# Performance work log

Measured on AMD Instinct MI355X. Metric: run time of the kernel, lower is better.

The kernel has to match this reference:

```python
import jax, jax.numpy as jnp
import numpy as np

B, S, D = 2, 2048, 1024
H = 16
HEAD_DIM = 64          # matches head_dim init arg; D // H == 64
HALF_WINDOW = 32       # local_window_size // 2
SCALE = HEAD_DIM ** -0.5


def setup_inputs() -> dict:
    key = jax.random.key(0)
    ks = jax.random.split(key, 6)
    std = 1.0 / np.sqrt(D)
    return {
        "x": jax.random.normal(ks[0], (B, S, D), dtype=jnp.float32),
        "Wq": jax.random.normal(ks[1], (D, D), dtype=jnp.float32) * std,
        "Wk": jax.random.normal(ks[2], (D, D), dtype=jnp.float32) * std,
        "Wv": jax.random.normal(ks[3], (D, D), dtype=jnp.float32) * std,
        "Wo": jax.random.normal(ks[4], (D, D), dtype=jnp.float32) * std,
        "bo": jnp.zeros((D,), dtype=jnp.float32),
    }


def reference(x, Wq, Wk, Wv, Wo, bo):
    b, s, d = x.shape
    h, hd = H, d // H

    def split_heads(y):  # [b, s, d] -> [b, h, s, hd]
        return y.reshape(b, s, h, hd).transpose(0, 2, 1, 3)

    q = split_heads(x @ Wq) * SCALE
    k = split_heads(x @ Wk)
    v = split_heads(x @ Wv)

    # dense scores [b, h, s, s] (module materializes full O(S^2) matrix)
    scores = jnp.einsum("bhqd,bhkd->bhqk", q, k)

    # local window |i-j| <= HALF_WINDOW combined with causal j <= i
    i = jnp.arange(s)
    local = jnp.abs(i[:, None] - i[None, :]) <= HALF_WINDOW
    causal = i[None, :] <= i[:, None]
    mask = local & causal  # [s, s]
    scores = jnp.where(mask[None, None, :, :], scores, -jnp.inf)

    attn = jax.nn.softmax(scores, axis=-1)  # diagonal always valid -> no NaN
    out = jnp.einsum("bhqk,bhkd->bhqd", attn, v)
    out = out.transpose(0, 2, 1, 3).reshape(b, s, d)  # merge heads
    return out @ Wo + bo
```

## Files before the change

### kernel.cpp

```cpp
#include <hip/hip_runtime.h>
#include <hip/hip_bf16.h>

typedef __bf16 bf16_t;
typedef __bf16 bf16x8 __attribute__((ext_vector_type(8)));
typedef __bf16 bf16x4 __attribute__((ext_vector_type(4)));
typedef float  f32x4  __attribute__((ext_vector_type(4)));

#define B_   2
#define S_   2048
#define D_   1024
#define H_   16
#define HD_  64
#define HW   32
#define SCALE_ 0.125f

__device__ __forceinline__ void gl_lds16(const bf16_t* g, bf16_t* l) {
  __builtin_amdgcn_global_load_lds(
      (const __attribute__((address_space(1))) void*)g,
      (__attribute__((address_space(3))) void*)l, 16, 0, 0);
}

__global__ __launch_bounds__(256) void k_conv(const float* __restrict__ X,
                                              const float* __restrict__ W0,
                                              const float* __restrict__ W1,
                                              const float* __restrict__ W2,
                                              const float* __restrict__ W3,
                                              bf16_t* __restrict__ Xb,
                                              bf16_t* __restrict__ Wt) {
  __shared__ bf16_t t[64][72];
  int bid = blockIdx.x;
  int tid = threadIdx.x;
  if (bid < 2048) {
    int i = bid * 256 + tid;
    const float4 a = ((const float4*)X)[i * 2];
    const float4 b = ((const float4*)X)[i * 2 + 1];
    bf16x8 r;
    r[0] = (bf16_t)a.x; r[1] = (bf16_t)a.y; r[2] = (bf16_t)a.z; r[3] = (bf16_t)a.w;
    r[4] = (bf16_t)b.x; r[5] = (bf16_t)b.y; r[6] = (bf16_t)b.z; r[7] = (bf16_t)b.w;
    ((bf16x8*)Xb)[i] = r;
    return;
  }
  int wb = bid - 2048;
  int wsel = wb >> 8;
  const float* W = (wsel == 0) ? W0 : (wsel == 1) ? W1 : (wsel == 2) ? W2 : W3;
  bf16_t* dst = Wt + (size_t)wsel * D_ * D_;
  int tile = wb & 255;
  int k0 = (tile >> 4) * 64, n0 = (tile & 15) * 64;
  int r = tid >> 4, c4 = (tid & 15) * 4;
#pragma unroll
  for (int i = 0; i < 4; ++i) {
    int row = i * 16 + r;
    float4 v = *(const float4*)(W + (size_t)(k0 + row) * D_ + n0 + c4);
    t[row][c4 + 0] = (bf16_t)v.x;
    t[row][c4 + 1] = (bf16_t)v.y;
    t[row][c4 + 2] = (bf16_t)v.z;
    t[row][c4 + 3] = (bf16_t)v.w;
  }
  __syncthreads();
#pragma unroll
  for (int i = 0; i < 4; ++i) {
    int row = i * 16 + r;
    bf16x4 o;
    o[0] = t[c4 + 0][row];
    o[1] = t[c4 + 1][row];
    o[2] = t[c4 + 2][row];
    o[3] = t[c4 + 3][row];
    *(bf16x4*)(dst + (size_t)(n0 + row) * D_ + k0 + c4) = o;
  }
}

__global__ __launch_bounds__(256) void k_gemm_qkv(const bf16_t* __restrict__ X,
                                                  const bf16_t* __restrict__ Wt,
                                                  bf16_t* __restrict__ Q,
                                                  bf16_t* __restrict__ K,
                                                  bf16_t* __restrict__ V) {
  __shared__ bf16_t sA[128 * 32];
  __shared__ bf16_t sB[128 * 32];
  int bid = blockIdx.x;
  int mt = bid & 31, nt = bid >> 5;
  int wsel = nt >> 3;
  int n0 = (nt & 7) * 128, m0 = mt * 128;
  const bf16_t* Wp = Wt + (size_t)wsel * D_ * D_;
  int tid = threadIdx.x, lane = tid & 63, wave = tid >> 6;
  int wr = (wave >> 1) * 64, wc = (wave & 1) * 64;
  int r0 = wave * 32 + (lane >> 2);
  int ce = (lane & 3) * 8;
  const bf16_t* gA0 = X + (size_t)(m0 + r0) * D_ + ce;
  const bf16_t* gB0 = Wp + (size_t)(n0 + r0) * D_ + ce;
  bf16_t* lA0 = sA + wave * 1024;
  bf16_t* lB0 = sB + wave * 1024;
  f32x4 acc[4][4] = {};
  int kq = (lane >> 4) * 8, rl = lane & 15;
  for (int kt = 0; kt < D_; kt += 32) {
    __syncthreads();
    gl_lds16(gA0 + kt, lA0);
    gl_lds16(gA0 + kt + (size_t)16 * D_, lA0 + 512);
    gl_lds16(gB0 + kt, lB0);
    gl_lds16(gB0 + kt + (size_t)16 * D_, lB0 + 512);
    __syncthreads();
    bf16x8 af[4], bfr[4];
#pragma unroll
    for (int m = 0; m < 4; ++m)
      af[m] = *(const bf16x8*)&sA[(wr + m * 16 + rl) * 32 + kq];
#pragma unroll
    for (int n = 0; n < 4; ++n)
      bfr[n] = *(const bf16x8*)&sB[(wc + n * 16 + rl) * 32 + kq];
#pragma unroll
    for (int m = 0; m < 4; ++m)
#pragma unroll
      for (int n = 0; n < 4; ++n)
        acc[m][n] = __builtin_amdgcn_mfma_f32_16x16x32_bf16(af[m], bfr[n], acc[m][n], 0, 0, 0);
  }
  float qscale = (wsel == 0) ? SCALE_ : 1.0f;
#pragma unroll
  for (int m = 0; m < 4; ++m) {
#pragma unroll
    for (int n = 0; n < 4; ++n) {
#pragma unroll
      for (int r = 0; r < 4; ++r) {
        int gm = m0 + wr + m * 16 + (lane >> 4) * 4 + r;
        int gn = n0 + wc + n * 16 + rl;
        int b = gm >> 11, s = gm & 2047;
        int h = gn >> 6, hd = gn & 63;
        bf16_t val = (bf16_t)(acc[m][n][r] * qscale);
        if (wsel == 0)
          Q[(((size_t)(b * H_ + h)) * S_ + s) * HD_ + hd] = val;
        else if (wsel == 1)
          K[(((size_t)(b * H_ + h)) * S_ + s) * HD_ + hd] = val;
        else
          V[(((size_t)(b * H_ + h)) * HD_ + hd) * S_ + s] = val;
      }
    }
  }
}

__global__ __launch_bounds__(256) void k_gemm_out(const bf16_t* __restrict__ A,
                                                  const bf16_t* __restrict__ Wp,
                                                  const float* __restrict__ bo,
                                                  float* __restrict__ out) {
  __shared__ bf16_t sA[64 * 32];
  __shared__ bf16_t sB[128 * 32];
  int bid = blockIdx.x;
  int mt = bid & 63, nt = bid >> 6;
  int n0 = nt * 128, m0 = mt * 64;
  int tid = threadIdx.x, lane = tid & 63, wave = tid >> 6;
  int wc = wave * 32;
  int crow = lane >> 2, ccol = (lane & 3) * 8;
  const bf16_t* gsrc0; bf16_t* ldst0;
  const bf16_t* gsrc1; bf16_t* ldst1;
  const bf16_t* gsrc2; bf16_t* ldst2;
#pragma unroll
  for (int j = 0; j < 3; ++j) {
    int c = wave * 3 + j;
    const bf16_t* g; bf16_t* l;
    if (c < 4) {
      g = A + (size_t)(m0 + c * 16 + crow) * D_ + ccol;
      l = sA + c * 512;
    } else {
      g = Wp + (size_t)(n0 + (c - 4) * 16 + crow) * D_ + ccol;
      l = sB + (c - 4) * 512;
    }
    if (j == 0) { gsrc0 = g; ldst0 = l; }
    else if (j == 1) { gsrc1 = g; ldst1 = l; }
    else { gsrc2 = g; ldst2 = l; }
  }
  f32x4 acc[4][2] = {};
  int kq = (lane >> 4) * 8, rl = lane & 15, hi = lane >> 4;
  for (int kt = 0; kt < D_; kt += 32) {
    __syncthreads();
    gl_lds16(gsrc0 + kt, ldst0);
    gl_lds16(gsrc1 + kt, ldst1);
    gl_lds16(gsrc2 + kt, ldst2);
    __syncthreads();
    bf16x8 af[4], bfr[2];
#pragma unroll
    for (int m = 0; m < 4; ++m)
      af[m] = *(const bf16x8*)&sA[(m * 16 + rl) * 32 + kq];
#pragma unroll
    for (int n = 0; n < 2; ++n)
      bfr[n] = *(const bf16x8*)&sB[(wc + n * 16 + rl) * 32 + kq];
#pragma unroll
    for (int m = 0; m < 4; ++m)
#pragma unroll
      for (int n = 0; n < 2; ++n)
        acc[m][n] = __builtin_amdgcn_mfma_f32_16x16x32_bf16(af[m], bfr[n], acc[m][n], 0, 0, 0);
  }
#pragma unroll
  for (int m = 0; m < 4; ++m) {
#pragma unroll
    for (int n = 0; n < 2; ++n) {
#pragma unroll
      for (int r = 0; r < 4; ++r) {
        int gm = m0 + m * 16 + hi * 4 + r;
        int gn = n0 + wc + n * 16 + rl;
        out[(size_t)gm * D_ + gn] = acc[m][n][r] + bo[gn];
      }
    }
  }
}

#define QB 64
#define KW 112
#define KLP 68
#define VTP 116

__global__ __launch_bounds__(256) void k_attn(const bf16_t* __restrict__ Q,
                                              const bf16_t* __restrict__ K,
                                              const bf16_t* __restrict__ Vt,
                                              bf16_t* __restrict__ O) {
  __shared__ bf16_t sK[KW][KLP];
  __shared__ bf16_t sV[HD_][VTP];
  __shared__ bf16_t sP[4][16][KLP];
  int bid = blockIdx.x;
  int qb = bid & 31, bh = bid >> 5;
  int q0 = qb * QB;
  const bf16_t* Kp = K + (size_t)bh * S_ * HD_;
  const bf16_t* Vp = Vt + (size_t)bh * HD_ * S_;
  const bf16_t* Qp = Q + (size_t)bh * S_ * HD_;
  int tid = threadIdx.x;
  int lane = tid & 63, wave = tid >> 6;
  int rl = lane & 15, hi = lane >> 4;
  int wk0b = q0 - HW;
  bf16x8 qf0 = *(const bf16x8*)(Qp + (size_t)(q0 + wave * 16 + rl) * HD_ + hi * 8);
  bf16x8 qf1 = *(const bf16x8*)(Qp + (size_t)(q0 + wave * 16 + rl) * HD_ + 32 + hi * 8);
  for (int idx = tid; idx < KW * 8; idx += 256) {
    int row = idx >> 3, c8 = (idx & 7) * 8;
    int kg = wk0b + row;
    kg = kg < 0 ? 0 : (kg > S_ - 1 ? S_ - 1 : kg);
    *(bf16x8*)&sK[row][c8] = *(const bf16x8*)(Kp + (size_t)kg * HD_ + c8);
  }
  for (int idx = tid; idx < HD_ * 14; idx += 256) {
    int row = idx / 14, c8 = (idx % 14) * 8;
    int ks = wk0b + c8;
    ks = ks < 0 ? 0 : (ks > S_ - 8 ? S_ - 8 : ks);
    *(bf16x8*)&sV[row][c8] = *(const bf16x8*)(Vp + (size_t)row * S_ + ks);
  }
  __syncthreads();
  int wko = wave * 16;
  f32x4 accs[4] = {};
#pragma unroll
  for (int kb = 0; kb < 4; ++kb) {
    bf16x8 kf = *(const bf16x8*)&sK[wko + kb * 16 + rl][hi * 8];
    accs[kb] = __builtin_amdgcn_mfma_f32_16x16x32_bf16(kf, qf0, accs[kb], 0, 0, 0);
  }
#pragma unroll
  for (int kb = 0; kb < 4; ++kb) {
    bf16x8 kf = *(const bf16x8*)&sK[wko + kb * 16 + rl][32 + hi * 8];
    accs[kb] = __builtin_amdgcn_mfma_f32_16x16x32_bf16(kf, qf1, accs[kb], 0, 0, 0);
  }
  float p[4][4];
  float mx = -1e30f;
#pragma unroll
  for (int kb = 0; kb < 4; ++kb) {
#pragma unroll
    for (int r = 0; r < 4; ++r) {
      int kl = kb * 16 + hi * 4 + r;
      bool valid = (kl >= rl) && (kl <= rl + HW) && (wk0b + wko + kl >= 0);
      float s = valid ? accs[kb][r] : -1e30f;
      p[kb][r] = s;
      mx = fmaxf(mx, s);
    }
  }
  mx = fmaxf(mx, __shfl_xor(mx, 16));
  mx = fmaxf(mx, __shfl_xor(mx, 32));
  float sum = 0.f;
#pragma unroll
  for (int kb = 0; kb < 4; ++kb)
#pragma unroll
    for (int r = 0; r < 4; ++r) {
      p[kb][r] = __expf(p[kb][r] - mx);
      sum += p[kb][r];
    }
  sum += __shfl_xor(sum, 16);
  sum += __shfl_xor(sum, 32);
  float inv = 1.f / sum;
#pragma unroll
  for (int kb = 0; kb < 4; ++kb) {
    bf16x4 pv;
#pragma unroll
    for (int r = 0; r < 4; ++r) pv[r] = (bf16_t)(p[kb][r] * inv);
    *(bf16x4*)&sP[wave][rl][kb * 16 + hi * 4] = pv;
  }
  f32x4 acco[4] = {};
#pragma unroll
  for (int ks = 0; ks < 2; ++ks) {
    bf16x8 aP = *(const bf16x8*)&sP[wave][rl][ks * 32 + hi * 8];
#pragma unroll
    for (int n = 0; n < 4; ++n) {
      bf16x8 bV = *(const bf16x8*)&sV[n * 16 + rl][wko + ks * 32 + hi * 8];
      acco[n] = __builtin_amdgcn_mfma_f32_16x16x32_bf16(aP, bV, acco[n], 0, 0, 0);
    }
  }
  int b = bh >> 4, h = bh & 15;
#pragma unroll
  for (int n = 0; n < 4; ++n) {
#pragma unroll
    for (int r = 0; r < 4; ++r) {
      int qgl = q0 + wave * 16 + hi * 4 + r;
      int d = n * 16 + rl;
      O[((size_t)(b * S_ + qgl)) * D_ + h * HD_ + d] = (bf16_t)acco[n][r];
    }
  }
}

extern "C" void kernel_launch(void* const* d_in, const int* in_sizes, int n_in,
                              void* d_out, int out_size, void* d_ws, size_t ws_size,
                              hipStream_t stream) {
  const float* x  = (const float*)d_in[0];
  const float* Wq = (const float*)d_in[1];
  const float* Wk = (const float*)d_in[2];
  const float* Wv = (const float*)d_in[3];
  const float* Wo = (const float*)d_in[4];
  const float* bo = (const float*)d_in[5];
  float* out = (float*)d_out;
  char* ws = (char*)d_ws;
  bf16_t* xb = (bf16_t*)(ws);
  bf16_t* wt = (bf16_t*)(ws + (size_t)(8 << 20));
  bf16_t* qb = (bf16_t*)(ws + (size_t)(16 << 20));
  bf16_t* kb = (bf16_t*)(ws + (size_t)(24 << 20));
  bf16_t* vb = (bf16_t*)(ws + (size_t)(32 << 20));
  bf16_t* ob = (bf16_t*)(ws + (size_t)(40 << 20));

  hipLaunchKernelGGL(k_conv, dim3(3072), dim3(256), 0, stream,
                     x, Wq, Wk, Wv, Wo, xb, wt);
  hipLaunchKernelGGL(k_gemm_qkv, dim3(768), dim3(256), 0, stream, xb, wt, qb, kb, vb);
  hipLaunchKernelGGL(k_attn, dim3(1024), dim3(256), 0, stream, qb, kb, vb, ob);
  hipLaunchKernelGGL(k_gemm_out, dim3(512), dim3(256), 0, stream,
                     ob, wt + (size_t)3 * D_ * D_, bo, out);
}
```

Measured before the change: 81.50 us.

## Rewrite QKV GEMM with triple-buffered async LDS pipeline and swizzled layout

The QKV projection GEMM moves to 512-thread blocks with 128x192 tiles spanning the fused Q/K/V weight, a K-step of 64, and a three-stage global-to-LDS async pipeline synchronised through explicit vmcnt waits and barriers. LDS rows are XOR-swizzled to avoid bank conflicts, and MFMA issue runs at raised wave priority. This targets exposed load latency and the two barriers per 32-wide K step of the old loop. In exchange it uses much more LDS (about 120KB), which limits blocks per CU, and the hand-coded waitcnt counts are fragile.

```diff
diff --git a/kernel.cpp b/kernel.cpp
--- a/kernel.cpp
+++ b/kernel.cpp
@@ -69,64 +69,107 @@
   }
 }
 
-__global__ __launch_bounds__(256) void k_gemm_qkv(const bf16_t* __restrict__ X,
+__global__ __launch_bounds__(512) void k_gemm_qkv(const bf16_t* __restrict__ X,
                                                   const bf16_t* __restrict__ Wt,
                                                   bf16_t* __restrict__ Q,
-                                                  bf16_t* __restrict__ K,
+                                                  bf16_t* __restrict__ Kb,
                                                   bf16_t* __restrict__ V) {
-  __shared__ bf16_t sA[128 * 32];
-  __shared__ bf16_t sB[128 * 32];
+  __shared__ bf16_t sA[3 * 128 * 64];
+  __shared__ bf16_t sB[3 * 192 * 64];
   int bid = blockIdx.x;
   int mt = bid & 31, nt = bid >> 5;
-  int wsel = nt >> 3;
-  int n0 = (nt & 7) * 128, m0 = mt * 128;
-  const bf16_t* Wp = Wt + (size_t)wsel * D_ * D_;
+  int m0 = mt * 128, n0g = nt * 192;
   int tid = threadIdx.x, lane = tid & 63, wave = tid >> 6;
-  int wr = (wave >> 1) * 64, wc = (wave & 1) * 64;
-  int r0 = wave * 32 + (lane >> 2);
-  int ce = (lane & 3) * 8;
-  const bf16_t* gA0 = X + (size_t)(m0 + r0) * D_ + ce;
-  const bf16_t* gB0 = Wp + (size_t)(n0 + r0) * D_ + ce;
-  bf16_t* lA0 = sA + wave * 1024;
-  bf16_t* lB0 = sB + wave * 1024;
-  f32x4 acc[4][4] = {};
-  int kq = (lane >> 4) * 8, rl = lane & 15;
-  for (int kt = 0; kt < D_; kt += 32) {
-    __syncthreads();
-    gl_lds16(gA0 + kt, lA0);
-    gl_lds16(gA0 + kt + (size_t)16 * D_, lA0 + 512);
-    gl_lds16(gB0 + kt, lB0);
-    gl_lds16(gB0 + kt + (size_t)16 * D_, lB0 + 512);
-    __syncthreads();
-    bf16x8 af[4], bfr[4];
-#pragma unroll
-    for (int m = 0; m < 4; ++m)
-      af[m] = *(const bf16x8*)&sA[(wr + m * 16 + rl) * 32 + kq];
-#pragma unroll
-    for (int n = 0; n < 4; ++n)
-      bfr[n] = *(const bf16x8*)&sB[(wc + n * 16 + rl) * 32 + kq];
-#pragma unroll
-    for (int m = 0; m < 4; ++m)
-#pragma unroll
-      for (int n = 0; n < 4; ++n)
-        acc[m][n] = __builtin_amdgcn_mfma_f32_16x16x32_bf16(af[m], bfr[n], acc[m][n], 0, 0, 0);
-  }
-  float qscale = (wsel == 0) ? SCALE_ : 1.0f;
+  int wm = wave >> 2, wn = wave & 3;
+  int srow8 = lane >> 3, sc16 = (lane & 7) ^ srow8;
+  int rl = lane & 15, hi = lane >> 4, r7 = rl & 7;
+  const bf16_t* gst0; const bf16_t* gst1; const bf16_t* gst2;
+  const bf16_t* gst3; const bf16_t* gst4;
+  int lst0, lst1, lst2, lst3, lst4;
+  {
+    int c0 = wave,     c1 = 8 + wave;
+    gst0 = X + (size_t)(m0 + c0 * 8 + srow8) * D_ + sc16 * 8;  lst0 = c0 * 512;
+    gst1 = X + (size_t)(m0 + c1 * 8 + srow8) * D_ + sc16 * 8;  lst1 = c1 * 512;
+    int b0 = wave, b1 = 8 + wave, b2 = 16 + wave;
+    gst2 = Wt + (size_t)(n0g + b0 * 8 + srow8) * D_ + sc16 * 8; lst2 = b0 * 512;
+    gst3 = Wt + (size_t)(n0g + b1 * 8 + srow8) * D_ + sc16 * 8; lst3 = b1 * 512;
+    gst4 = Wt + (size_t)(n0g + b2 * 8 + srow8) * D_ + sc16 * 8; lst4 = b2 * 512;
+  }
+#define STAGE_(bi, kt) do { \
+    gl_lds16(gst0 + (kt), sA + (bi) * 8192 + lst0);  \
+    gl_lds16(gst1 + (kt), sA + (bi) * 8192 + lst1);  \
+    gl_lds16(gst2 + (kt), sB + (bi) * 12288 + lst2); \
+    gl_lds16(gst3 + (kt), sB + (bi) * 12288 + lst3); \
+    gl_lds16(gst4 + (kt), sB + (bi) * 12288 + lst4); \
+  } while (0)
+  f32x4 acc[4][3] = {};
+  STAGE_(0, 0);
+  STAGE_(1, 64);
+  asm volatile("s_waitcnt vmcnt(5)" ::: "memory");
+  __builtin_amdgcn_sched_barrier(0);
+  __builtin_amdgcn_s_barrier();
+  asm volatile("" ::: "memory");
+  int cur = 0;
+  for (int t = 0; t < 16; ++t) {
+    const bf16_t* pA = sA + cur * 8192;
+    const bf16_t* pB = sB + cur * 12288;
+    bf16x8 af[4][2], bfr[3][2];
+#pragma unroll
+    for (int m = 0; m < 4; ++m) {
+      int rr = (wm * 64 + m * 16 + rl) * 64;
+#pragma unroll
+      for (int kk = 0; kk < 2; ++kk)
+        af[m][kk] = *(const bf16x8*)&pA[rr + ((kk * 4 + hi) ^ r7) * 8];
+    }
+#pragma unroll
+    for (int n = 0; n < 3; ++n) {
+      int rr = (wn * 48 + n * 16 + rl) * 64;
+#pragma unroll
+      for (int kk = 0; kk < 2; ++kk)
+        bfr[n][kk] = *(const bf16x8*)&pB[rr + ((kk * 4 + hi) ^ r7) * 8];
+    }
+    int sb = cur + 2; if (sb >= 3) sb -= 3;
+    if (t + 2 < 16) STAGE_(sb, (t + 2) * 64);
+    __builtin_amdgcn_s_setprio(1);
+#pragma unroll
+    for (int kk = 0; kk < 2; ++kk)
+#pragma unroll
+      for (int m = 0; m < 4; ++m)
+#pragma unroll
+        for (int n = 0; n < 3; ++n)
+          acc[m][n] = __builtin_amdgcn_mfma_f32_16x16x32_bf16(af[m][kk], bfr[n][kk], acc[m][n], 0, 0, 0);
+    __builtin_amdgcn_s_setprio(0);
+    if (t < 14) {
+      asm volatile("s_waitcnt vmcnt(5)" ::: "memory");
+    } else if (t == 14) {
+      asm volatile("s_waitcnt vmcnt(0)" ::: "memory");
+    }
+    if (t < 15) {
+      __builtin_amdgcn_sched_barrier(0);
+      __builtin_amdgcn_s_barrier();
+      asm volatile("" ::: "memory");
+    }
+    if (++cur == 3) cur = 0;
+  }
+#undef STAGE_
 #pragma unroll
   for (int m = 0; m < 4; ++m) {
-#pragma unroll
-    for (int n = 0; n < 4; ++n) {
+    int gm = m0 + wm * 64 + m * 16 + hi * 4;
+#pragma unroll
+    for (int n = 0; n < 3; ++n) {
+      int gn = n0g + wn * 48 + n * 16 + rl;
+      int wsel = gn >> 10, col = gn & 1023;
+      int h = col >> 6, hd = col & 63;
+      float qs = (wsel == 0) ? SCALE_ : 1.0f;
 #pragma unroll
       for (int r = 0; r < 4; ++r) {
-        int gm = m0 + wr + m * 16 + (lane >> 4) * 4 + r;
-        int gn = n0 + wc + n * 16 + rl;
-        int b = gm >> 11, s = gm & 2047;
-        int h = gn >> 6, hd = gn & 63;
-        bf16_t val = (bf16_t)(acc[m][n][r] * qscale);
+        int gmr = gm + r;
+        int b = gmr >> 11, s = gmr & 2047;
+        bf16_t val = (bf16_t)(acc[m][n][r] * qs);
         if (wsel == 0)
           Q[(((size_t)(b * H_ + h)) * S_ + s) * HD_ + hd] = val;
         else if (wsel == 1)
-          K[(((size_t)(b * H_ + h)) * S_ + s) * HD_ + hd] = val;
+          Kb[(((size_t)(b * H_ + h)) * S_ + s) * HD_ + hd] = val;
         else
           V[(((size_t)(b * H_ + h)) * HD_ + hd) * S_ + s] = val;
       }
@@ -323,7 +366,7 @@
 
   hipLaunchKernelGGL(k_conv, dim3(3072), dim3(256), 0, stream,
                      x, Wq, Wk, Wv, Wo, xb, wt);
-  hipLaunchKernelGGL(k_gemm_qkv, dim3(768), dim3(256), 0, stream, xb, wt, qb, kb, vb);
+  hipLaunchKernelGGL(k_gemm_qkv, dim3(512), dim3(512), 0, stream, xb, wt, qb, kb, vb);
   hipLaunchKernelGGL(k_attn, dim3(1024), dim3(256), 0, stream, qb, kb, vb, ob);
   hipLaunchKernelGGL(k_gemm_out, dim3(512), dim3(256), 0, stream,
                      ob, wt + (size_t)3 * D_ * D_, bo, out);
```

Result: slower. 83.56 us (+2.5%).

## Triple-buffer QKV GEMM LDS loads with async prefetch and one barrier per step

Applied to the files above, without the earlier changes.

The QKV projection GEMM now keeps three LDS stages and issues direct global-to-LDS loads two k-steps ahead. Per iteration it waits on vmcnt and uses a single barrier instead of two full syncthreads. MFMA issue is raised in priority with s_setprio. This aims to hide global-load latency behind MFMA work, at the cost of triple the LDS footprint (48KB per block), which may lower occupancy.

```diff
diff --git a/kernel.cpp b/kernel.cpp
--- a/kernel.cpp
+++ b/kernel.cpp
@@ -72,10 +72,10 @@
 __global__ __launch_bounds__(256) void k_gemm_qkv(const bf16_t* __restrict__ X,
                                                   const bf16_t* __restrict__ Wt,
                                                   bf16_t* __restrict__ Q,
-                                                  bf16_t* __restrict__ K,
+                                                  bf16_t* __restrict__ Kb,
                                                   bf16_t* __restrict__ V) {
-  __shared__ bf16_t sA[128 * 32];
-  __shared__ bf16_t sB[128 * 32];
+  __shared__ bf16_t sA[3 * 128 * 32];
+  __shared__ bf16_t sB[3 * 128 * 32];
   int bid = blockIdx.x;
   int mt = bid & 31, nt = bid >> 5;
   int wsel = nt >> 3;
@@ -87,30 +87,54 @@
   int ce = (lane & 3) * 8;
   const bf16_t* gA0 = X + (size_t)(m0 + r0) * D_ + ce;
   const bf16_t* gB0 = Wp + (size_t)(n0 + r0) * D_ + ce;
-  bf16_t* lA0 = sA + wave * 1024;
-  bf16_t* lB0 = sB + wave * 1024;
+  int lofs = wave * 1024;
+#define QSTAGE_(bi, kt) do { \
+    gl_lds16(gA0 + (kt), sA + (bi) * 4096 + lofs);        \
+    gl_lds16(gA0 + (kt) + (size_t)16 * D_, sA + (bi) * 4096 + lofs + 512); \
+    gl_lds16(gB0 + (kt), sB + (bi) * 4096 + lofs);        \
+    gl_lds16(gB0 + (kt) + (size_t)16 * D_, sB + (bi) * 4096 + lofs + 512); \
+  } while (0)
   f32x4 acc[4][4] = {};
   int kq = (lane >> 4) * 8, rl = lane & 15;
-  for (int kt = 0; kt < D_; kt += 32) {
-    __syncthreads();
-    gl_lds16(gA0 + kt, lA0);
-    gl_lds16(gA0 + kt + (size_t)16 * D_, lA0 + 512);
-    gl_lds16(gB0 + kt, lB0);
-    gl_lds16(gB0 + kt + (size_t)16 * D_, lB0 + 512);
-    __syncthreads();
+  QSTAGE_(0, 0);
+  QSTAGE_(1, 32);
+  asm volatile("s_waitcnt vmcnt(4)" ::: "memory");
+  __builtin_amdgcn_sched_barrier(0);
+  __builtin_amdgcn_s_barrier();
+  asm volatile("" ::: "memory");
+  int cur = 0;
+  for (int t = 0; t < 32; ++t) {
+    const bf16_t* pA = sA + cur * 4096;
+    const bf16_t* pB = sB + cur * 4096;
     bf16x8 af[4], bfr[4];
 #pragma unroll
     for (int m = 0; m < 4; ++m)
-      af[m] = *(const bf16x8*)&sA[(wr + m * 16 + rl) * 32 + kq];
+      af[m] = *(const bf16x8*)&pA[(wr + m * 16 + rl) * 32 + kq];
 #pragma unroll
     for (int n = 0; n < 4; ++n)
-      bfr[n] = *(const bf16x8*)&sB[(wc + n * 16 + rl) * 32 + kq];
+      bfr[n] = *(const bf16x8*)&pB[(wc + n * 16 + rl) * 32 + kq];
+    int sb = cur + 2; if (sb >= 3) sb -= 3;
+    if (t + 2 < 32) QSTAGE_(sb, (t + 2) * 32);
+    __builtin_amdgcn_s_setprio(1);
 #pragma unroll
     for (int m = 0; m < 4; ++m)
 #pragma unroll
       for (int n = 0; n < 4; ++n)
         acc[m][n] = __builtin_amdgcn_mfma_f32_16x16x32_bf16(af[m], bfr[n], acc[m][n], 0, 0, 0);
-  }
+    __builtin_amdgcn_s_setprio(0);
+    if (t < 30) {
+      asm volatile("s_waitcnt vmcnt(4)" ::: "memory");
+    } else if (t == 30) {
+      asm volatile("s_waitcnt vmcnt(0)" ::: "memory");
+    }
+    if (t < 31) {
+      __builtin_amdgcn_sched_barrier(0);
+      __builtin_amdgcn_s_barrier();
+      asm volatile("" ::: "memory");
+    }
+    if (++cur == 3) cur = 0;
+  }
+#undef QSTAGE_
   float qscale = (wsel == 0) ? SCALE_ : 1.0f;
 #pragma unroll
   for (int m = 0; m < 4; ++m) {
@@ -126,7 +150,7 @@
         if (wsel == 0)
           Q[(((size_t)(b * H_ + h)) * S_ + s) * HD_ + hd] = val;
         else if (wsel == 1)
-          K[(((size_t)(b * H_ + h)) * S_ + s) * HD_ + hd] = val;
+          Kb[(((size_t)(b * H_ + h)) * S_ + s) * HD_ + hd] = val;
         else
           V[(((size_t)(b * H_ + h)) * HD_ + hd) * S_ + s] = val;
       }
```

After: 81.71 us. No clear change (+0.2%).
